# Optimization experiments

Hardware: AMD Instinct MI355X
Metric: run time of the kernel (lower is better)

The kernel has to match this reference:

```python
import jax, jax.numpy as jnp
import numpy as np

NUM_HEADS = 16
WINDOW = 256  # window_size; tokens attend iff |i-j| <= WINDOW//2
LN_EPS = 1e-5


def setup_inputs() -> dict:
    key = jax.random.key(0)
    k1, k2, k3 = jax.random.split(key, 3)
    B, L, D = 2, 2048, 1024
    x = jax.random.normal(k1, (B, L, D), dtype=jnp.float32)
    w_qkv = jax.random.normal(k2, (3 * D, D), dtype=jnp.float32) * 0.02
    w_out = jax.random.normal(k3, (D, D), dtype=jnp.float32) * 0.02
    gamma = jnp.ones((D,), dtype=jnp.float32)
    beta = jnp.zeros((D,), dtype=jnp.float32)
    return {"x": x, "w_qkv": w_qkv, "w_out": w_out, "gamma": gamma, "beta": beta}


def reference(x, w_qkv, w_out, gamma, beta):
    B, L, D = x.shape
    H = NUM_HEADS
    HD = D // H
    residual = x
    # LayerNorm
    mu = jnp.mean(x, axis=-1, keepdims=True)
    var = jnp.mean(jnp.square(x - mu), axis=-1, keepdims=True)
    xn = (x - mu) * jax.lax.rsqrt(var + LN_EPS) * gamma + beta
    # QKV projection (torch Linear: y = x @ W.T)
    qkv = jnp.einsum('bld,ed->ble', xn, w_qkv).reshape(B, L, 3, H, HD)
    qkv = jnp.transpose(qkv, (2, 0, 3, 1, 4))  # [3, B, H, L, HD]
    q, k, v = qkv[0], qkv[1], qkv[2]
    # Dense scores with banded window mask (same math as the torch module)
    scores = jnp.einsum('bhqd,bhkd->bhqk', q, k) / jnp.sqrt(jnp.float32(HD))
    idx = jnp.arange(L)
    band = jnp.abs(idx[:, None] - idx[None, :]) <= (WINDOW // 2)  # [L, L] bool
    scores = jnp.where(band[None, None], scores, -jnp.inf)
    attn = jax.nn.softmax(scores, axis=-1)
    out = jnp.einsum('bhqk,bhkd->bhqd', attn, v)  # [B, H, L, HD]
    out = jnp.transpose(out, (0, 2, 1, 3)).reshape(B, L, D)
    return residual + jnp.einsum('bld,ed->ble', out, w_out)
```

## Files before the change

### kernel.cpp

```cpp
#include <hip/hip_runtime.h>

typedef unsigned int u32;
typedef unsigned short u16;
typedef __attribute__((ext_vector_type(8))) short short8;
typedef __attribute__((ext_vector_type(4))) float f32x4;

#define LSEQ 2048
#define DM 1024
#define HWIN 128

__device__ __forceinline__ u16 f2bf(float f) {
  union { float f; u32 u; } v; v.f = f;
  u32 r = v.u + 0x7FFFu + ((v.u >> 16) & 1u);
  return (u16)(r >> 16);
}
__device__ __forceinline__ u32 packbf(float lo, float hi) {
  return (u32)f2bf(lo) | ((u32)f2bf(hi) << 16);
}

typedef __attribute__((address_space(3))) u32 lds_u32;
typedef __attribute__((address_space(1))) const u32 glob_u32;
__device__ __forceinline__ void g2lds16(const void* g, void* l) {
  __builtin_amdgcn_global_load_lds((glob_u32*)g, (lds_u32*)l, 16, 0, 0);
}

__global__ __launch_bounds__(256) void ln_cvt_kernel(const float* __restrict__ x,
                                                     const float* __restrict__ gamma,
                                                     const float* __restrict__ beta,
                                                     u16* __restrict__ xn,
                                                     const float* __restrict__ wqi,
                                                     const float* __restrict__ woi,
                                                     u16* __restrict__ wq,
                                                     u16* __restrict__ wo) {
  int blk = blockIdx.x;
  int t = threadIdx.x;
  if (blk >= 4096) {
    const float* in; u16* out; int i;
    if (blk < 7168) { in = wqi; out = wq; i = (blk - 4096) * 256 + t; }
    else            { in = woi; out = wo; i = (blk - 7168) * 256 + t; }
    float4 v = ((const float4*)in)[i];
    u32* dst = (u32*)out + i * 2;
    dst[0] = packbf(v.x, v.y);
    dst[1] = packbf(v.z, v.w);
    return;
  }
  int r = blk;
  const float4* xr = (const float4*)(x + (size_t)r * DM);
  float4 v = xr[t];
  float s = v.x + v.y + v.z + v.w;
  float s2 = v.x * v.x + v.y * v.y + v.z * v.z + v.w * v.w;
#pragma unroll
  for (int o = 32; o; o >>= 1) { s += __shfl_xor(s, o); s2 += __shfl_xor(s2, o); }
  __shared__ float ws1[4], ws2[4];
  if ((t & 63) == 0) { ws1[t >> 6] = s; ws2[t >> 6] = s2; }
  __syncthreads();
  s = ws1[0] + ws1[1] + ws1[2] + ws1[3];
  s2 = ws2[0] + ws2[1] + ws2[2] + ws2[3];
  float mu = s * (1.0f / DM);
  float var = s2 * (1.0f / DM) - mu * mu;
  float rs = rsqrtf(var + 1e-5f);
  float4 g = ((const float4*)gamma)[t];
  float4 b = ((const float4*)beta)[t];
  u32 lo = packbf((v.x - mu) * rs * g.x + b.x, (v.y - mu) * rs * g.y + b.y);
  u32 hi = packbf((v.z - mu) * rs * g.z + b.z, (v.w - mu) * rs * g.w + b.w);
  u32* dst = (u32*)(xn + (size_t)r * DM) + t * 2;
  dst[0] = lo; dst[1] = hi;
}

__device__ __forceinline__ void stage_tile(const u16* __restrict__ G, int gr0, int K,
                                           int k0, u16* lbuf, int tid, int w) {
#pragma unroll
  for (int j = 0; j < 4; ++j) {
    int rp = j * 32 + (tid >> 3);
    int ce = ((tid & 7) ^ (rp & 7)) * 8;
    g2lds16(G + (size_t)(gr0 + rp) * K + k0 + ce, lbuf + j * 2048 + w * 512);
  }
}

template <int MODE>
__global__ __launch_bounds__(256) void gemm_bt(const u16* __restrict__ Ag,
                                               const u16* __restrict__ Bg,
                                               int K, int NB,
                                               u16* __restrict__ qk_out,
                                               u16* __restrict__ vt_out,
                                               const float* __restrict__ resid,
                                               float* __restrict__ out) {
  __shared__ __align__(16) u16 sm[32768];
  int tid = threadIdx.x;
  int w = tid >> 6, l = tid & 63;
  int lg = l >> 4, li = l & 15;
  int bm = blockIdx.x / NB, bn = blockIdx.x % NB;
  int wr = w >> 1, wc = w & 1;
  f32x4 acc[4][4];
#pragma unroll
  for (int m = 0; m < 4; ++m)
#pragma unroll
    for (int n = 0; n < 4; ++n) acc[m][n] = (f32x4){0.f, 0.f, 0.f, 0.f};

  int nt = K >> 6;
  stage_tile(Ag, bm * 128, K, 0, sm, tid, w);
  stage_tile(Bg, bn * 128, K, 0, sm + 8192, tid, w);
  asm volatile("s_waitcnt vmcnt(0)" ::: "memory");
  __builtin_amdgcn_s_barrier();
  asm volatile("" ::: "memory");

  int cur = 0;
  for (int t = 0; t < nt; ++t) {
    if (t + 1 < nt) {
      stage_tile(Ag, bm * 128, K, (t + 1) << 6, sm + (cur ^ 1) * 16384, tid, w);
      stage_tile(Bg, bn * 128, K, (t + 1) << 6, sm + (cur ^ 1) * 16384 + 8192, tid, w);
    }
    const u16* Ab = sm + cur * 16384;
    const u16* Bb = Ab + 8192;
#pragma unroll
    for (int ks = 0; ks < 2; ++ks) {
      short8 af[4], bf4[4];
#pragma unroll
      for (int m = 0; m < 4; ++m)
        af[m] = *(const short8*)&Ab[(wr * 64 + m * 16 + li) * 64 + (((lg + ks * 4) ^ (li & 7)) * 8)];
#pragma unroll
      for (int n = 0; n < 4; ++n)
        bf4[n] = *(const short8*)&Bb[(wc * 64 + n * 16 + li) * 64 + (((lg + ks * 4) ^ (li & 7)) * 8)];
#pragma unroll
      for (int m = 0; m < 4; ++m)
#pragma unroll
        for (int n = 0; n < 4; ++n)
          acc[m][n] = __builtin_amdgcn_mfma_f32_16x16x32_bf16(af[m], bf4[n], acc[m][n], 0, 0, 0);
    }
    asm volatile("s_waitcnt vmcnt(0)" ::: "memory");
    __builtin_amdgcn_s_barrier();
    asm volatile("" ::: "memory");
    cur ^= 1;
  }

  int colbase = bn * 128 + wc * 64;
  int rowbase = bm * 128 + wr * 64;
#pragma unroll
  for (int m = 0; m < 4; ++m) {
    int row = rowbase + m * 16 + lg * 4;
#pragma unroll
    for (int n = 0; n < 4; ++n) {
      int col = colbase + n * 16 + li;
      if (MODE == 0) {
        if (colbase < 2048) {
#pragma unroll
          for (int r = 0; r < 4; ++r)
            qk_out[(size_t)(row + r) * 2048 + col] = f2bf(acc[m][n][r]);
        } else {
          int b = row >> 11;
          int hdcol = col - 2048;
          size_t idx = ((size_t)b * 1024 + hdcol) * 2048 + (row & 2047);
          u32* d = (u32*)&vt_out[idx];
          d[0] = packbf(acc[m][n][0], acc[m][n][1]);
          d[1] = packbf(acc[m][n][2], acc[m][n][3]);
        }
      } else {
#pragma unroll
        for (int r = 0; r < 4; ++r) {
          size_t idx = (size_t)(row + r) * 1024 + col;
          out[idx] = resid[idx] + acc[m][n][r];
        }
      }
    }
  }
}

__global__ __launch_bounds__(256) void attn_kernel(const u16* __restrict__ qk,
                                                   const u16* __restrict__ vt,
                                                   u16* __restrict__ ato) {
  int blk0 = blockIdx.x;
  int xcd = blk0 & 7;
  int j = blk0 >> 3;
  int bh = xcd * 4 + (j & 3);
  int qblk = j >> 2;
  int b = bh >> 4, h = bh & 15;
  int tid = threadIdx.x;
  int w = tid >> 6, l = tid & 63;
  int pair = w >> 1, half = w & 1;
  int lg = l >> 4, li = l & 15;
  int qw = qblk * 32 + pair * 16;
  int q = qw + li;
  int sg0 = (((2 * lg) & 3) << 4) + li;
  int sg1 = (((2 * lg + 1) & 3) << 4) + li;

  const u16* qbase = qk + (size_t)(b * 2048 + q) * 2048 + h * 64 + lg * 8;
  short8 qf0 = *(const short8*)qbase;
  short8 qf1 = *(const short8*)(qbase + 32);

  const u16* kbase = qk + (size_t)b * 2048 * 2048 + 1024 + h * 64 + lg * 8;
  const u16* vbase = vt + (size_t)(bh * 64 + li) * 2048;

  f32x4 o0 = {0,0,0,0}, o1 = {0,0,0,0}, o2 = {0,0,0,0}, o3 = {0,0,0,0};
  float mrun = -1e30f, lsum = 0.f;

  int lo = qw - HWIN; if (lo < 0) lo = 0;
  int hi = qw + 15 + HWIN; if (hi > LSEQ - 1) hi = LSEQ - 1;
  int kb0 = lo & ~31;
  int n = ((hi - kb0) >> 5) + 1;
  const float SC = 0.125f * 1.44269504088896f;

  for (int c = half; c < n; c += 2) {
    int kb = kb0 + (c << 5);
    const u16* kp0 = kbase + (size_t)(kb + li) * 2048;
    const u16* kp1 = kp0 + (size_t)16 * 2048;
    short8 k00 = *(const short8*)kp0;
    short8 k01 = *(const short8*)(kp0 + 32);
    short8 k10 = *(const short8*)kp1;
    short8 k11 = *(const short8*)(kp1 + 32);
    f32x4 c0 = {0,0,0,0}, c1 = {0,0,0,0};
    c0 = __builtin_amdgcn_mfma_f32_16x16x32_bf16(k00, qf0, c0, 0, 0, 0);
    c0 = __builtin_amdgcn_mfma_f32_16x16x32_bf16(k01, qf1, c0, 0, 0, 0);
    c1 = __builtin_amdgcn_mfma_f32_16x16x32_bf16(k10, qf0, c1, 0, 0, 0);
    c1 = __builtin_amdgcn_mfma_f32_16x16x32_bf16(k11, qf1, c1, 0, 0, 0);

    float t[8];
    bool interior = (kb >= qw + 15 - HWIN) && (kb + 31 <= qw + HWIN);
    if (interior) {
#pragma unroll
      for (int r = 0; r < 4; ++r) { t[r] = c0[r] * SC; t[r + 4] = c1[r] * SC; }
    } else {
#pragma unroll
      for (int r = 0; r < 4; ++r) {
        int key0 = kb + lg * 4 + r;
        int key1 = key0 + 16;
        int d0 = key0 - q, d1 = key1 - q;
        t[r]     = (d0 >= -HWIN && d0 <= HWIN) ? c0[r] * SC : -__builtin_inff();
        t[r + 4] = (d1 >= -HWIN && d1 <= HWIN) ? c1[r] * SC : -__builtin_inff();
      }
    }
    float mA = fmaxf(fmaxf(t[0], t[1]), fmaxf(t[2], t[3]));
    float mB = fmaxf(fmaxf(t[4], t[5]), fmaxf(t[6], t[7]));
    float mc = fmaxf(mA, mB);
    mc = fmaxf(mc, __shfl_xor(mc, 16));
    mc = fmaxf(mc, __shfl_xor(mc, 32));

    float p[8];
    if (__all(mc <= mrun + 8.0f)) {
      float s0 = 0.f;
#pragma unroll
      for (int i = 0; i < 8; ++i) { p[i] = __builtin_amdgcn_exp2f(t[i] - mrun); s0 += p[i]; }
      lsum += s0;
    } else {
      float mn = fmaxf(mrun, mc);
      float corr = __builtin_amdgcn_exp2f(mrun - mn);
      float s0 = 0.f;
#pragma unroll
      for (int i = 0; i < 8; ++i) { p[i] = __builtin_amdgcn_exp2f(t[i] - mn); s0 += p[i]; }
      lsum = lsum * corr + s0;
      mrun = mn;
      o0 *= corr; o1 *= corr; o2 *= corr; o3 *= corr;
    }

    u32 a0 = packbf(p[0], p[1]);
    u32 a1 = packbf(p[2], p[3]);
    u32 b0 = packbf(p[4], p[5]);
    u32 b1 = packbf(p[6], p[7]);
    u32 w0 = (u32)__shfl((int)a0, sg0), w1 = (u32)__shfl((int)a1, sg0);
    u32 w2 = (u32)__shfl((int)a0, sg1), w3 = (u32)__shfl((int)a1, sg1);
    u32 x0 = (u32)__shfl((int)b0, sg0), x1 = (u32)__shfl((int)b1, sg0);
    u32 x2 = (u32)__shfl((int)b0, sg1), x3 = (u32)__shfl((int)b1, sg1);
    bool lohalf = lg < 2;
    union { u32 u[4]; short8 s; } pf;
    pf.u[0] = lohalf ? w0 : x0;
    pf.u[1] = lohalf ? w1 : x1;
    pf.u[2] = lohalf ? w2 : x2;
    pf.u[3] = lohalf ? w3 : x3;

    const u16* vp = vbase + kb + lg * 8;
    short8 v0 = *(const short8*)(vp);
    short8 v1 = *(const short8*)(vp + (size_t)16 * 2048);
    short8 v2 = *(const short8*)(vp + (size_t)32 * 2048);
    short8 v3 = *(const short8*)(vp + (size_t)48 * 2048);
    o0 = __builtin_amdgcn_mfma_f32_16x16x32_bf16(v0, pf.s, o0, 0, 0, 0);
    o1 = __builtin_amdgcn_mfma_f32_16x16x32_bf16(v1, pf.s, o1, 0, 0, 0);
    o2 = __builtin_amdgcn_mfma_f32_16x16x32_bf16(v2, pf.s, o2, 0, 0, 0);
    o3 = __builtin_amdgcn_mfma_f32_16x16x32_bf16(v3, pf.s, o3, 0, 0, 0);
  }

  lsum += __shfl_xor(lsum, 16);
  lsum += __shfl_xor(lsum, 32);

  __shared__ float ml[2][2][2][16];
  __shared__ float olds[2][64][18];
  if (l < 16) { ml[pair][half][0][li] = mrun; ml[pair][half][1][li] = lsum; }
  __syncthreads();
  float m0 = ml[pair][0][0][li], l0 = ml[pair][0][1][li];
  float m1 = ml[pair][1][0][li], l1 = ml[pair][1][1][li];
  float ms = fmaxf(m0, m1);
  float c0s = __builtin_amdgcn_exp2f(m0 - ms);
  float c1s = __builtin_amdgcn_exp2f(m1 - ms);
  float ltot = l0 * c0s + l1 * c1s;
  float myc = half ? c1s : c0s;
  o0 *= myc; o1 *= myc; o2 *= myc; o3 *= myc;

  if (half == 1) {
#pragma unroll
    for (int r = 0; r < 4; ++r) {
      olds[pair][ 0 + lg * 4 + r][li] = o0[r];
      olds[pair][16 + lg * 4 + r][li] = o1[r];
      olds[pair][32 + lg * 4 + r][li] = o2[r];
      olds[pair][48 + lg * 4 + r][li] = o3[r];
    }
  }
  __syncthreads();
  if (half == 0) {
#pragma unroll
    for (int r = 0; r < 4; ++r) {
      o0[r] += olds[pair][ 0 + lg * 4 + r][li];
      o1[r] += olds[pair][16 + lg * 4 + r][li];
      o2[r] += olds[pair][32 + lg * 4 + r][li];
      o3[r] += olds[pair][48 + lg * 4 + r][li];
    }
    float inv = 1.0f / ltot;
    u16* orow = ato + (size_t)(b * 2048 + q) * 1024 + h * 64 + lg * 4;
    *(u32*)(orow +  0) = packbf(o0[0] * inv, o0[1] * inv);
    *(u32*)(orow +  2) = packbf(o0[2] * inv, o0[3] * inv);
    *(u32*)(orow + 16) = packbf(o1[0] * inv, o1[1] * inv);
    *(u32*)(orow + 18) = packbf(o1[2] * inv, o1[3] * inv);
    *(u32*)(orow + 32) = packbf(o2[0] * inv, o2[1] * inv);
    *(u32*)(orow + 34) = packbf(o2[2] * inv, o2[3] * inv);
    *(u32*)(orow + 48) = packbf(o3[0] * inv, o3[1] * inv);
    *(u32*)(orow + 50) = packbf(o3[2] * inv, o3[3] * inv);
  }
}

extern "C" void kernel_launch(void* const* d_in, const int* in_sizes, int n_in,
                              void* d_out, int out_size, void* d_ws, size_t ws_size,
                              hipStream_t stream) {
  const float* x     = (const float*)d_in[0];
  const float* w_qkv = (const float*)d_in[1];
  const float* w_out = (const float*)d_in[2];
  const float* gamma = (const float*)d_in[3];
  const float* beta  = (const float*)d_in[4];
  float* out = (float*)d_out;
  char* ws = (char*)d_ws;

  u16* xn  = (u16*)(ws);
  u16* wq  = (u16*)(ws + 8388608);
  u16* wo  = (u16*)(ws + 14680064);
  u16* qkb = (u16*)(ws + 16777216);
  u16* vt  = (u16*)(ws + 33554432);
  u16* ao  = (u16*)(ws + 41943040);

  ln_cvt_kernel<<<8192, 256, 0, stream>>>(x, gamma, beta, xn, w_qkv, w_out, wq, wo);
  gemm_bt<0><<<32 * 24, 256, 0, stream>>>(xn, wq, 1024, 24, qkb, vt, nullptr, nullptr);
  attn_kernel<<<32 * 64, 256, 0, stream>>>(qkb, vt, ao);
  gemm_bt<1><<<32 * 8, 256, 0, stream>>>(ao, wo, 1024, 8, nullptr, nullptr, x, out);
}
```

Before: 105.2 us.

## Restructure attention warps, fold Q scaling into GEMM, use hardware bf16 pack

Several changes at once. Float-to-bf16 conversion now uses the v_cvt_pk_bf16_f32 instruction instead of manual rounding. The softmax scale is folded into the Q epilogue of the QKV GEMM. The QKV GEMM becomes a persistent grid-stride loop over 768 tiles with 512 blocks. The attention kernel drops its two-wave key split and LDS merge: each wave now handles 16 queries over the full window using 16x16x16 MFMAs with no P shuffles, and the grid halves to 1024 blocks. This removes the cross-wave reduction and barriers, but gives fewer, longer-running waves and an uneven tile count per block in the persistent GEMM.

```diff
diff --git a/kernel.cpp b/kernel.cpp
--- a/kernel.cpp
+++ b/kernel.cpp
@@ -3,19 +3,18 @@
 typedef unsigned int u32;
 typedef unsigned short u16;
 typedef __attribute__((ext_vector_type(8))) short short8;
+typedef __attribute__((ext_vector_type(4))) short short4v;
 typedef __attribute__((ext_vector_type(4))) float f32x4;
 
 #define LSEQ 2048
 #define DM 1024
 #define HWIN 128
-
-__device__ __forceinline__ u16 f2bf(float f) {
-  union { float f; u32 u; } v; v.f = f;
-  u32 r = v.u + 0x7FFFu + ((v.u >> 16) & 1u);
-  return (u16)(r >> 16);
-}
-__device__ __forceinline__ u32 packbf(float lo, float hi) {
-  return (u32)f2bf(lo) | ((u32)f2bf(hi) << 16);
+#define QSCALE 0.1803368801111204f
+
+__device__ __forceinline__ u32 pk(float lo, float hi) {
+  u32 r;
+  asm("v_cvt_pk_bf16_f32 %0, %1, %2" : "=v"(r) : "v"(lo), "v"(hi));
+  return r;
 }
 
 typedef __attribute__((address_space(3))) u32 lds_u32;
@@ -40,8 +39,8 @@
     else            { in = woi; out = wo; i = (blk - 7168) * 256 + t; }
     float4 v = ((const float4*)in)[i];
     u32* dst = (u32*)out + i * 2;
-    dst[0] = packbf(v.x, v.y);
-    dst[1] = packbf(v.z, v.w);
+    dst[0] = pk(v.x, v.y);
+    dst[1] = pk(v.z, v.w);
     return;
   }
   int r = blk;
@@ -61,10 +60,9 @@
   float rs = rsqrtf(var + 1e-5f);
   float4 g = ((const float4*)gamma)[t];
   float4 b = ((const float4*)beta)[t];
-  u32 lo = packbf((v.x - mu) * rs * g.x + b.x, (v.y - mu) * rs * g.y + b.y);
-  u32 hi = packbf((v.z - mu) * rs * g.z + b.z, (v.w - mu) * rs * g.w + b.w);
   u32* dst = (u32*)(xn + (size_t)r * DM) + t * 2;
-  dst[0] = lo; dst[1] = hi;
+  dst[0] = pk((v.x - mu) * rs * g.x + b.x, (v.y - mu) * rs * g.y + b.y);
+  dst[1] = pk((v.z - mu) * rs * g.z + b.z, (v.w - mu) * rs * g.w + b.w);
 }
 
 __device__ __forceinline__ void stage_tile(const u16* __restrict__ G, int gr0, int K,
@@ -80,7 +78,7 @@
 template <int MODE>
 __global__ __launch_bounds__(256) void gemm_bt(const u16* __restrict__ Ag,
                                                const u16* __restrict__ Bg,
-                                               int K, int NB,
+                                               int K, int NB, int NT,
                                                u16* __restrict__ qk_out,
                                                u16* __restrict__ vt_out,
                                                const float* __restrict__ resid,
@@ -89,76 +87,83 @@
   int tid = threadIdx.x;
   int w = tid >> 6, l = tid & 63;
   int lg = l >> 4, li = l & 15;
-  int bm = blockIdx.x / NB, bn = blockIdx.x % NB;
   int wr = w >> 1, wc = w & 1;
-  f32x4 acc[4][4];
-#pragma unroll
-  for (int m = 0; m < 4; ++m)
-#pragma unroll
-    for (int n = 0; n < 4; ++n) acc[m][n] = (f32x4){0.f, 0.f, 0.f, 0.f};
-
-  int nt = K >> 6;
-  stage_tile(Ag, bm * 128, K, 0, sm, tid, w);
-  stage_tile(Bg, bn * 128, K, 0, sm + 8192, tid, w);
-  asm volatile("s_waitcnt vmcnt(0)" ::: "memory");
-  __builtin_amdgcn_s_barrier();
-  asm volatile("" ::: "memory");
-
-  int cur = 0;
-  for (int t = 0; t < nt; ++t) {
-    if (t + 1 < nt) {
-      stage_tile(Ag, bm * 128, K, (t + 1) << 6, sm + (cur ^ 1) * 16384, tid, w);
-      stage_tile(Bg, bn * 128, K, (t + 1) << 6, sm + (cur ^ 1) * 16384 + 8192, tid, w);
-    }
-    const u16* Ab = sm + cur * 16384;
-    const u16* Bb = Ab + 8192;
-#pragma unroll
-    for (int ks = 0; ks < 2; ++ks) {
-      short8 af[4], bf4[4];
-#pragma unroll
-      for (int m = 0; m < 4; ++m)
-        af[m] = *(const short8*)&Ab[(wr * 64 + m * 16 + li) * 64 + (((lg + ks * 4) ^ (li & 7)) * 8)];
-#pragma unroll
-      for (int n = 0; n < 4; ++n)
-        bf4[n] = *(const short8*)&Bb[(wc * 64 + n * 16 + li) * 64 + (((lg + ks * 4) ^ (li & 7)) * 8)];
-#pragma unroll
-      for (int m = 0; m < 4; ++m)
-#pragma unroll
-        for (int n = 0; n < 4; ++n)
-          acc[m][n] = __builtin_amdgcn_mfma_f32_16x16x32_bf16(af[m], bf4[n], acc[m][n], 0, 0, 0);
-    }
+
+  for (int tile = blockIdx.x; tile < NT; tile += gridDim.x) {
+    int bm = tile / NB, bn = tile % NB;
+    f32x4 acc[4][4];
+#pragma unroll
+    for (int m = 0; m < 4; ++m)
+#pragma unroll
+      for (int n = 0; n < 4; ++n) acc[m][n] = (f32x4){0.f, 0.f, 0.f, 0.f};
+
+    int nt = K >> 6;
+    stage_tile(Ag, bm * 128, K, 0, sm, tid, w);
+    stage_tile(Bg, bn * 128, K, 0, sm + 8192, tid, w);
     asm volatile("s_waitcnt vmcnt(0)" ::: "memory");
     __builtin_amdgcn_s_barrier();
     asm volatile("" ::: "memory");
-    cur ^= 1;
-  }
-
-  int colbase = bn * 128 + wc * 64;
-  int rowbase = bm * 128 + wr * 64;
-#pragma unroll
-  for (int m = 0; m < 4; ++m) {
-    int row = rowbase + m * 16 + lg * 4;
-#pragma unroll
-    for (int n = 0; n < 4; ++n) {
-      int col = colbase + n * 16 + li;
-      if (MODE == 0) {
-        if (colbase < 2048) {
-#pragma unroll
-          for (int r = 0; r < 4; ++r)
-            qk_out[(size_t)(row + r) * 2048 + col] = f2bf(acc[m][n][r]);
+
+    int cur = 0;
+    for (int t = 0; t < nt; ++t) {
+      if (t + 1 < nt) {
+        stage_tile(Ag, bm * 128, K, (t + 1) << 6, sm + (cur ^ 1) * 16384, tid, w);
+        stage_tile(Bg, bn * 128, K, (t + 1) << 6, sm + (cur ^ 1) * 16384 + 8192, tid, w);
+      }
+      const u16* Ab = sm + cur * 16384;
+      const u16* Bb = Ab + 8192;
+#pragma unroll
+      for (int ks = 0; ks < 2; ++ks) {
+        short8 af[4], bf4[4];
+#pragma unroll
+        for (int m = 0; m < 4; ++m)
+          af[m] = *(const short8*)&Ab[(wr * 64 + m * 16 + li) * 64 + (((lg + ks * 4) ^ (li & 7)) * 8)];
+#pragma unroll
+        for (int n = 0; n < 4; ++n)
+          bf4[n] = *(const short8*)&Bb[(wc * 64 + n * 16 + li) * 64 + (((lg + ks * 4) ^ (li & 7)) * 8)];
+#pragma unroll
+        for (int m = 0; m < 4; ++m)
+#pragma unroll
+          for (int n = 0; n < 4; ++n)
+            acc[m][n] = __builtin_amdgcn_mfma_f32_16x16x32_bf16(af[m], bf4[n], acc[m][n], 0, 0, 0);
+      }
+      asm volatile("s_waitcnt vmcnt(0)" ::: "memory");
+      __builtin_amdgcn_s_barrier();
+      asm volatile("" ::: "memory");
+      cur ^= 1;
+    }
+
+    int colbase = bn * 128 + wc * 64;
+    int rowbase = bm * 128 + wr * 64;
+#pragma unroll
+    for (int m = 0; m < 4; ++m) {
+      int row = rowbase + m * 16 + lg * 4;
+#pragma unroll
+      for (int n = 0; n < 4; ++n) {
+        int col = colbase + n * 16 + li;
+        if (MODE == 0) {
+          if (colbase < 2048) {
+            float qs = (colbase < 1024) ? QSCALE : 1.0f;
+            u32 p01 = pk(acc[m][n][0] * qs, acc[m][n][1] * qs);
+            u32 p23 = pk(acc[m][n][2] * qs, acc[m][n][3] * qs);
+            qk_out[(size_t)(row + 0) * 2048 + col] = (u16)p01;
+            qk_out[(size_t)(row + 1) * 2048 + col] = (u16)(p01 >> 16);
+            qk_out[(size_t)(row + 2) * 2048 + col] = (u16)p23;
+            qk_out[(size_t)(row + 3) * 2048 + col] = (u16)(p23 >> 16);
+          } else {
+            int b = row >> 11;
+            int hdcol = col - 2048;
+            size_t idx = ((size_t)b * 1024 + hdcol) * 2048 + (row & 2047);
+            u32* d = (u32*)&vt_out[idx];
+            d[0] = pk(acc[m][n][0], acc[m][n][1]);
+            d[1] = pk(acc[m][n][2], acc[m][n][3]);
+          }
         } else {
-          int b = row >> 11;
-          int hdcol = col - 2048;
-          size_t idx = ((size_t)b * 1024 + hdcol) * 2048 + (row & 2047);
-          u32* d = (u32*)&vt_out[idx];
-          d[0] = packbf(acc[m][n][0], acc[m][n][1]);
-          d[1] = packbf(acc[m][n][2], acc[m][n][3]);
-        }
-      } else {
-#pragma unroll
-        for (int r = 0; r < 4; ++r) {
-          size_t idx = (size_t)(row + r) * 1024 + col;
-          out[idx] = resid[idx] + acc[m][n][r];
+#pragma unroll
+          for (int r = 0; r < 4; ++r) {
+            size_t idx = (size_t)(row + r) * 1024 + col;
+            out[idx] = resid[idx] + acc[m][n][r];
+          }
         }
       }
     }
@@ -176,12 +181,9 @@
   int b = bh >> 4, h = bh & 15;
   int tid = threadIdx.x;
   int w = tid >> 6, l = tid & 63;
-  int pair = w >> 1, half = w & 1;
   int lg = l >> 4, li = l & 15;
-  int qw = qblk * 32 + pair * 16;
+  int qw = qblk * 64 + w * 16;
   int q = qw + li;
-  int sg0 = (((2 * lg) & 3) << 4) + li;
-  int sg1 = (((2 * lg + 1) & 3) << 4) + li;
 
   const u16* qbase = qk + (size_t)(b * 2048 + q) * 2048 + h * 64 + lg * 8;
   short8 qf0 = *(const short8*)qbase;
@@ -190,16 +192,17 @@
   const u16* kbase = qk + (size_t)b * 2048 * 2048 + 1024 + h * 64 + lg * 8;
   const u16* vbase = vt + (size_t)(bh * 64 + li) * 2048;
 
-  f32x4 o0 = {0,0,0,0}, o1 = {0,0,0,0}, o2 = {0,0,0,0}, o3 = {0,0,0,0};
+  f32x4 oo[4];
+#pragma unroll
+  for (int m = 0; m < 4; ++m) oo[m] = (f32x4){0.f, 0.f, 0.f, 0.f};
   float mrun = -1e30f, lsum = 0.f;
 
   int lo = qw - HWIN; if (lo < 0) lo = 0;
   int hi = qw + 15 + HWIN; if (hi > LSEQ - 1) hi = LSEQ - 1;
   int kb0 = lo & ~31;
   int n = ((hi - kb0) >> 5) + 1;
-  const float SC = 0.125f * 1.44269504088896f;
-
-  for (int c = half; c < n; c += 2) {
+
+  for (int c = 0; c < n; ++c) {
     int kb = kb0 + (c << 5);
     const u16* kp0 = kbase + (size_t)(kb + li) * 2048;
     const u16* kp1 = kp0 + (size_t)16 * 2048;
@@ -217,15 +220,15 @@
     bool interior = (kb >= qw + 15 - HWIN) && (kb + 31 <= qw + HWIN);
     if (interior) {
 #pragma unroll
-      for (int r = 0; r < 4; ++r) { t[r] = c0[r] * SC; t[r + 4] = c1[r] * SC; }
+      for (int r = 0; r < 4; ++r) { t[r] = c0[r]; t[r + 4] = c1[r]; }
     } else {
 #pragma unroll
       for (int r = 0; r < 4; ++r) {
         int key0 = kb + lg * 4 + r;
         int key1 = key0 + 16;
         int d0 = key0 - q, d1 = key1 - q;
-        t[r]     = (d0 >= -HWIN && d0 <= HWIN) ? c0[r] * SC : -__builtin_inff();
-        t[r + 4] = (d1 >= -HWIN && d1 <= HWIN) ? c1[r] * SC : -__builtin_inff();
+        t[r]     = (d0 >= -HWIN && d0 <= HWIN) ? c0[r] : -__builtin_inff();
+        t[r + 4] = (d1 >= -HWIN && d1 <= HWIN) ? c1[r] : -__builtin_inff();
       }
     }
     float mA = fmaxf(fmaxf(t[0], t[1]), fmaxf(t[2], t[3]));
@@ -248,79 +251,36 @@
       for (int i = 0; i < 8; ++i) { p[i] = __builtin_amdgcn_exp2f(t[i] - mn); s0 += p[i]; }
       lsum = lsum * corr + s0;
       mrun = mn;
-      o0 *= corr; o1 *= corr; o2 *= corr; o3 *= corr;
-    }
-
-    u32 a0 = packbf(p[0], p[1]);
-    u32 a1 = packbf(p[2], p[3]);
-    u32 b0 = packbf(p[4], p[5]);
-    u32 b1 = packbf(p[6], p[7]);
-    u32 w0 = (u32)__shfl((int)a0, sg0), w1 = (u32)__shfl((int)a1, sg0);
-    u32 w2 = (u32)__shfl((int)a0, sg1), w3 = (u32)__shfl((int)a1, sg1);
-    u32 x0 = (u32)__shfl((int)b0, sg0), x1 = (u32)__shfl((int)b1, sg0);
-    u32 x2 = (u32)__shfl((int)b0, sg1), x3 = (u32)__shfl((int)b1, sg1);
-    bool lohalf = lg < 2;
-    union { u32 u[4]; short8 s; } pf;
-    pf.u[0] = lohalf ? w0 : x0;
-    pf.u[1] = lohalf ? w1 : x1;
-    pf.u[2] = lohalf ? w2 : x2;
-    pf.u[3] = lohalf ? w3 : x3;
-
-    const u16* vp = vbase + kb + lg * 8;
-    short8 v0 = *(const short8*)(vp);
-    short8 v1 = *(const short8*)(vp + (size_t)16 * 2048);
-    short8 v2 = *(const short8*)(vp + (size_t)32 * 2048);
-    short8 v3 = *(const short8*)(vp + (size_t)48 * 2048);
-    o0 = __builtin_amdgcn_mfma_f32_16x16x32_bf16(v0, pf.s, o0, 0, 0, 0);
-    o1 = __builtin_amdgcn_mfma_f32_16x16x32_bf16(v1, pf.s, o1, 0, 0, 0);
-    o2 = __builtin_amdgcn_mfma_f32_16x16x32_bf16(v2, pf.s, o2, 0, 0, 0);
-    o3 = __builtin_amdgcn_mfma_f32_16x16x32_bf16(v3, pf.s, o3, 0, 0, 0);
+#pragma unroll
+      for (int m = 0; m < 4; ++m) oo[m] *= corr;
+    }
+
+    union { u32 u[2]; short4v s; } pb0, pb1;
+    pb0.u[0] = pk(p[0], p[1]); pb0.u[1] = pk(p[2], p[3]);
+    pb1.u[0] = pk(p[4], p[5]); pb1.u[1] = pk(p[6], p[7]);
+
+    short4v va[4][2];
+#pragma unroll
+    for (int m = 0; m < 4; ++m) {
+      va[m][0] = *(const short4v*)(vbase + (size_t)m * 32768 + kb + lg * 4);
+      va[m][1] = *(const short4v*)(vbase + (size_t)m * 32768 + kb + 16 + lg * 4);
+    }
+#pragma unroll
+    for (int m = 0; m < 4; ++m) {
+      asm("v_mfma_f32_16x16x16_bf16 %0, %1, %2, %0" : "+v"(oo[m]) : "v"(va[m][0]), "v"(pb0.s));
+      asm("v_mfma_f32_16x16x16_bf16 %0, %1, %2, %0" : "+v"(oo[m]) : "v"(va[m][1]), "v"(pb1.s));
+    }
   }
 
   lsum += __shfl_xor(lsum, 16);
   lsum += __shfl_xor(lsum, 32);
-
-  __shared__ float ml[2][2][2][16];
-  __shared__ float olds[2][64][18];
-  if (l < 16) { ml[pair][half][0][li] = mrun; ml[pair][half][1][li] = lsum; }
-  __syncthreads();
-  float m0 = ml[pair][0][0][li], l0 = ml[pair][0][1][li];
-  float m1 = ml[pair][1][0][li], l1 = ml[pair][1][1][li];
-  float ms = fmaxf(m0, m1);
-  float c0s = __builtin_amdgcn_exp2f(m0 - ms);
-  float c1s = __builtin_amdgcn_exp2f(m1 - ms);
-  float ltot = l0 * c0s + l1 * c1s;
-  float myc = half ? c1s : c0s;
-  o0 *= myc; o1 *= myc; o2 *= myc; o3 *= myc;
-
-  if (half == 1) {
-#pragma unroll
-    for (int r = 0; r < 4; ++r) {
-      olds[pair][ 0 + lg * 4 + r][li] = o0[r];
-      olds[pair][16 + lg * 4 + r][li] = o1[r];
-      olds[pair][32 + lg * 4 + r][li] = o2[r];
-      olds[pair][48 + lg * 4 + r][li] = o3[r];
-    }
-  }
-  __syncthreads();
-  if (half == 0) {
-#pragma unroll
-    for (int r = 0; r < 4; ++r) {
-      o0[r] += olds[pair][ 0 + lg * 4 + r][li];
-      o1[r] += olds[pair][16 + lg * 4 + r][li];
-      o2[r] += olds[pair][32 + lg * 4 + r][li];
-      o3[r] += olds[pair][48 + lg * 4 + r][li];
-    }
-    float inv = 1.0f / ltot;
-    u16* orow = ato + (size_t)(b * 2048 + q) * 1024 + h * 64 + lg * 4;
-    *(u32*)(orow +  0) = packbf(o0[0] * inv, o0[1] * inv);
-    *(u32*)(orow +  2) = packbf(o0[2] * inv, o0[3] * inv);
-    *(u32*)(orow + 16) = packbf(o1[0] * inv, o1[1] * inv);
-    *(u32*)(orow + 18) = packbf(o1[2] * inv, o1[3] * inv);
-    *(u32*)(orow + 32) = packbf(o2[0] * inv, o2[1] * inv);
-    *(u32*)(orow + 34) = packbf(o2[2] * inv, o2[3] * inv);
-    *(u32*)(orow + 48) = packbf(o3[0] * inv, o3[1] * inv);
-    *(u32*)(orow + 50) = packbf(o3[2] * inv, o3[3] * inv);
+  asm volatile("s_nop 7\n\ts_nop 7");
+  float inv = 1.0f / lsum;
+  u16* orow = ato + (size_t)(b * 2048 + q) * 1024 + h * 64 + lg * 4;
+#pragma unroll
+  for (int m = 0; m < 4; ++m) {
+    *(u32*)(orow + m * 16 + 0) = pk(oo[m][0] * inv, oo[m][1] * inv);
+    *(u32*)(orow + m * 16 + 2) = pk(oo[m][2] * inv, oo[m][3] * inv);
   }
 }
 
@@ -343,7 +303,7 @@
   u16* ao  = (u16*)(ws + 41943040);
 
   ln_cvt_kernel<<<8192, 256, 0, stream>>>(x, gamma, beta, xn, w_qkv, w_out, wq, wo);
-  gemm_bt<0><<<32 * 24, 256, 0, stream>>>(xn, wq, 1024, 24, qkb, vt, nullptr, nullptr);
-  attn_kernel<<<32 * 64, 256, 0, stream>>>(qkb, vt, ao);
-  gemm_bt<1><<<32 * 8, 256, 0, stream>>>(ao, wo, 1024, 8, nullptr, nullptr, x, out);
-}
+  gemm_bt<0><<<512, 256, 0, stream>>>(xn, wq, 1024, 24, 768, qkb, vt, nullptr, nullptr);
+  attn_kernel<<<1024, 256, 0, stream>>>(qkb, vt, ao);
+  gemm_bt<1><<<256, 256, 0, stream>>>(ao, wo, 1024, 8, 256, nullptr, nullptr, x, out);
+}
```

Result: slower. 120.2 us (+14.3%).
